# Kernel tuning notes

Hardware: AMD Instinct MI355X
Metric: run time of the kernel (lower is better)

The kernel has to match this reference:

```python
import jax, jax.numpy as jnp
import numpy as np

M, N = 8192, 8192
BITS = 3
BETA1, BETA2 = 16, 16
NNZ_PER_ROW = 32


def setup_inputs() -> dict:
    key = jax.random.key(0)
    ks = jax.random.split(key, 10)
    tm, tn = M // BETA1, N // BETA2
    nnz = M * NNZ_PER_ROW
    x = jax.random.normal(ks[0], (1, 10, N), dtype=jnp.float32)
    # quantized weight codes and first-order quantized scale/zero codes (3-bit)
    W = jax.random.randint(ks[1], (M, N), 0, 2 ** BITS, dtype=jnp.int32)
    W_s = jax.random.randint(ks[2], (M, tn), 0, 2 ** BITS, dtype=jnp.int32)
    W_z = jax.random.randint(ks[3], (M, tn), 0, 2 ** BITS, dtype=jnp.int32)
    # second-order (per-tile) float scale/zero for the quantized scales/zeros
    W_s_s = jax.random.uniform(ks[4], (tm, tn), jnp.float32, 0.01, 0.1)
    W_s_z = jax.random.uniform(ks[5], (tm, tn), jnp.float32, 0.0, 1.0)
    W_z_s = jax.random.uniform(ks[6], (tm, tn), jnp.float32, 0.01, 0.1)
    W_z_z = jax.random.uniform(ks[7], (tm, tn), jnp.float32, 0.0, 1.0)
    # CSR outliers: fixed 32 nnz per row
    row_offsets = jnp.arange(M + 1, dtype=jnp.int32) * NNZ_PER_ROW
    col_ids = jax.random.randint(ks[8], (nnz,), 0, N, dtype=jnp.int32)
    values = jax.random.normal(ks[9], (nnz,), dtype=jnp.float32)
    return dict(x=x, W=W, W_s=W_s, W_z=W_z, W_s_s=W_s_s, W_s_z=W_s_z,
                W_z_s=W_z_s, W_z_z=W_z_z, row_offsets=row_offsets,
                col_ids=col_ids, values=values)


def _dequantize(W, W_s, W_z, W_s_s, W_s_z, W_z_s, W_z_z):
    m, n = W.shape
    tm, tn = W_s_s.shape
    beta1, beta2 = m // tm, n // tn
    # two-level dequant: first-order scale/zero are themselves quantized per tile
    s = (W_s.astype(jnp.float32).reshape(tm, beta1, tn) - W_s_z[:, None, :]) * W_s_s[:, None, :]
    z = (W_z.astype(jnp.float32).reshape(tm, beta1, tn) - W_z_z[:, None, :]) * W_z_s[:, None, :]
    s = s.reshape(m, tn)  # (m, n/beta2)
    z = z.reshape(m, tn)
    w = (W.astype(jnp.float32).reshape(m, tn, beta2) - z[:, :, None]) * s[:, :, None]
    return w.reshape(m, n)


def reference(x, W, W_s, W_z, W_s_s, W_s_z, W_z_s, W_z_z, row_offsets, col_ids, values):
    Wd = _dequantize(W, W_s, W_z, W_s_s, W_s_z, W_z_s, W_z_z)  # (m, n)
    m = Wd.shape[0]
    b, l, n = x.shape
    xf = x.reshape(b * l, n)
    # dense quantized matmul: y = x @ Wd^T
    y = jnp.einsum('bn,mn->bm', xf, Wd)
    # CSR sparse outlier correction
    nnz = values.shape[0]
    rows = jnp.repeat(jnp.arange(m, dtype=jnp.int32), jnp.diff(row_offsets),
                      total_repeat_length=nnz)
    contrib = values[:, None] * xf[:, col_ids].T  # (nnz, B)
    y = y + jax.ops.segment_sum(contrib, rows, num_segments=m).T
    return y.reshape(b, l, m)
```

## Files before the change

### kernel.cpp

```cpp
#include <hip/hip_runtime.h>


constexpr int M_DIM = 8192;
constexpr int N_DIM = 8192;
constexpr int TN    = 512;
constexpr int BQ    = 10;
constexpr int RB    = 4;
constexpr int NTHREADS = 256;
constexpr int NC    = NTHREADS * 4;
constexpr int NCHUNK = N_DIM / NC;

__global__ __launch_bounds__(NTHREADS, 4)
void spqr_fused(const float* __restrict__ x,
                const int*   __restrict__ W,
                const int*   __restrict__ Ws,
                const int*   __restrict__ Wz,
                const float* __restrict__ Wss,
                const float* __restrict__ Wsz,
                const float* __restrict__ Wzs,
                const float* __restrict__ Wzz,
                const int*   __restrict__ row_offsets,
                const int*   __restrict__ col_ids,
                const float* __restrict__ values,
                float*       __restrict__ y)
{
    const int t  = threadIdx.x;
    const int m0 = blockIdx.x * RB;

    float acc[RB][BQ];
    #pragma unroll
    for (int r = 0; r < RB; ++r)
        #pragma unroll
        for (int b = 0; b < BQ; ++b)
            acc[r][b] = 0.f;

    for (int chunk = 0; chunk < NCHUNK; ++chunk) {
        const int n0 = chunk * NC + t * 4;
        float4 xv[BQ];
        #pragma unroll
        for (int b = 0; b < BQ; ++b)
            xv[b] = *reinterpret_cast<const float4*>(x + b * N_DIM + n0);

        const int g = n0 >> 4;

        #pragma unroll
        for (int r = 0; r < RB; ++r) {
            const int m  = m0 + r;
            const int ti = m >> 4;
            const int tIdx = ti * TN + g;
            const float s = ((float)Ws[m * TN + g] - Wsz[tIdx]) * Wss[tIdx];
            const float z = ((float)Wz[m * TN + g] - Wzz[tIdx]) * Wzs[tIdx];
            const int4 wc = *reinterpret_cast<const int4*>(W + (size_t)m * N_DIM + n0);
            const float w0 = ((float)wc.x - z) * s;
            const float w1 = ((float)wc.y - z) * s;
            const float w2 = ((float)wc.z - z) * s;
            const float w3 = ((float)wc.w - z) * s;
            #pragma unroll
            for (int b = 0; b < BQ; ++b) {
                float a = acc[r][b];
                a = fmaf(w0, xv[b].x, a);
                a = fmaf(w1, xv[b].y, a);
                a = fmaf(w2, xv[b].z, a);
                a = fmaf(w3, xv[b].w, a);
                acc[r][b] = a;
            }
        }
    }

    #pragma unroll
    for (int r = 0; r < RB; ++r)
        #pragma unroll
        for (int b = 0; b < BQ; ++b) {
            float v = acc[r][b];
            for (int off = 32; off > 0; off >>= 1)
                v += __shfl_xor(v, off, 64);
            acc[r][b] = v;
        }

    __shared__ float lds_part[NTHREADS / 64][RB * BQ];
    __shared__ float lds_sp[RB][BQ];

    const int wave = t >> 6;
    const int lane = t & 63;
    if (lane == 0) {
        #pragma unroll
        for (int r = 0; r < RB; ++r)
            #pragma unroll
            for (int b = 0; b < BQ; ++b)
                lds_part[wave][r * BQ + b] = acc[r][b];
    }
    if (t < RB * BQ)
        lds_sp[t / BQ][t % BQ] = 0.f;
    __syncthreads();

    if (t < RB * 32) {
        const int r = t >> 5;
        const int j = t & 31;
        const int m = m0 + r;
        const int base = row_offsets[m];
        const int cnt  = row_offsets[m + 1] - base;
        float c[BQ];
        #pragma unroll
        for (int b = 0; b < BQ; ++b) c[b] = 0.f;
        for (int jj = j; jj < cnt; jj += 32) {
            const int   col = col_ids[base + jj];
            const float v   = values[base + jj];
            #pragma unroll
            for (int b = 0; b < BQ; ++b)
                c[b] = fmaf(v, x[b * N_DIM + col], c[b]);
        }
        #pragma unroll
        for (int b = 0; b < BQ; ++b) {
            float v = c[b];
            for (int off = 16; off > 0; off >>= 1)
                v += __shfl_xor(v, off, 32);
            c[b] = v;
        }
        if (j == 0) {
            #pragma unroll
            for (int b = 0; b < BQ; ++b)
                lds_sp[r][b] = c[b];
        }
    }
    __syncthreads();

    if (t < RB * BQ) {
        const int r = t / BQ;
        const int b = t % BQ;
        float v = lds_sp[r][b];
        #pragma unroll
        for (int w = 0; w < NTHREADS / 64; ++w)
            v += lds_part[w][r * BQ + b];
        y[b * M_DIM + (m0 + r)] = v;
    }
}

extern "C" void kernel_launch(void* const* d_in, const int* in_sizes, int n_in,
                              void* d_out, int out_size, void* d_ws, size_t ws_size,
                              hipStream_t stream)
{
    const float* x    = (const float*)d_in[0];
    const int*   W    = (const int*)  d_in[1];
    const int*   Ws   = (const int*)  d_in[2];
    const int*   Wz   = (const int*)  d_in[3];
    const float* Wss  = (const float*)d_in[4];
    const float* Wsz  = (const float*)d_in[5];
    const float* Wzs  = (const float*)d_in[6];
    const float* Wzz  = (const float*)d_in[7];
    const int*   roff = (const int*)  d_in[8];
    const int*   cids = (const int*)  d_in[9];
    const float* vals = (const float*)d_in[10];
    float* yout = (float*)d_out;

    dim3 grid(M_DIM / RB);
    dim3 block(NTHREADS);
    spqr_fused<<<grid, block, 0, stream>>>(x, W, Ws, Wz, Wss, Wsz, Wzs, Wzz,
                                           roff, cids, vals, yout);
}
```

Baseline: 83.61 us.

## Process eight rows per block, hoist tile scales, restructure cross-thread reduction

Doubles the rows per block from 4 to 8 so each loaded x chunk is reused across more weight rows, and lowers the launch-bounds occupancy hint to allow more registers. Since 8 rows sit in one 16-row tile, the four second-order scale/zero loads are hoisted out of the row loop. The final reduction swaps the full 64-lane shuffle tree for a 2-step shuffle plus an LDS transpose reduction, and now all 256 threads run the sparse outlier pass. The cost is higher register pressure, lower occupancy, and half as many blocks.

```diff
diff --git a/kernel.cpp b/kernel.cpp
--- a/kernel.cpp
+++ b/kernel.cpp
@@ -5,12 +5,13 @@
 constexpr int N_DIM = 8192;
 constexpr int TN    = 512;
 constexpr int BQ    = 10;
-constexpr int RB    = 4;
+constexpr int RB    = 8;
 constexpr int NTHREADS = 256;
 constexpr int NC    = NTHREADS * 4;
 constexpr int NCHUNK = N_DIM / NC;
+constexpr int NOUT  = RB * BQ;
 
-__global__ __launch_bounds__(NTHREADS, 4)
+__global__ __launch_bounds__(NTHREADS, 2)
 void spqr_fused(const float* __restrict__ x,
                 const int*   __restrict__ W,
                 const int*   __restrict__ Ws,
@@ -26,6 +27,7 @@
 {
     const int t  = threadIdx.x;
     const int m0 = blockIdx.x * RB;
+    const int ti = m0 >> 4;
 
     float acc[RB][BQ];
     #pragma unroll
@@ -34,22 +36,29 @@
         for (int b = 0; b < BQ; ++b)
             acc[r][b] = 0.f;
 
+    const int tq = t * 4;
+
+    #pragma unroll 2
     for (int chunk = 0; chunk < NCHUNK; ++chunk) {
-        const int n0 = chunk * NC + t * 4;
+        const int n0 = chunk * NC + tq;
+        const int g  = n0 >> 4;
+        const int tIdx = ti * TN + g;
+
+        const float wss = Wss[tIdx];
+        const float wsz = Wsz[tIdx];
+        const float wzs = Wzs[tIdx];
+        const float wzz = Wzz[tIdx];
+
         float4 xv[BQ];
         #pragma unroll
         for (int b = 0; b < BQ; ++b)
             xv[b] = *reinterpret_cast<const float4*>(x + b * N_DIM + n0);
 
-        const int g = n0 >> 4;
-
         #pragma unroll
         for (int r = 0; r < RB; ++r) {
-            const int m  = m0 + r;
-            const int ti = m >> 4;
-            const int tIdx = ti * TN + g;
-            const float s = ((float)Ws[m * TN + g] - Wsz[tIdx]) * Wss[tIdx];
-            const float z = ((float)Wz[m * TN + g] - Wzz[tIdx]) * Wzs[tIdx];
+            const int m = m0 + r;
+            const float s = ((float)Ws[m * TN + g] - wsz) * wss;
+            const float z = ((float)Wz[m * TN + g] - wzz) * wzs;
             const int4 wc = *reinterpret_cast<const int4*>(W + (size_t)m * N_DIM + n0);
             const float w0 = ((float)wc.x - z) * s;
             const float w1 = ((float)wc.y - z) * s;
@@ -67,33 +76,8 @@
         }
     }
 
-    #pragma unroll
-    for (int r = 0; r < RB; ++r)
-        #pragma unroll
-        for (int b = 0; b < BQ; ++b) {
-            float v = acc[r][b];
-            for (int off = 32; off > 0; off >>= 1)
-                v += __shfl_xor(v, off, 64);
-            acc[r][b] = v;
-        }
-
-    __shared__ float lds_part[NTHREADS / 64][RB * BQ];
-    __shared__ float lds_sp[RB][BQ];
-
-    const int wave = t >> 6;
-    const int lane = t & 63;
-    if (lane == 0) {
-        #pragma unroll
-        for (int r = 0; r < RB; ++r)
-            #pragma unroll
-            for (int b = 0; b < BQ; ++b)
-                lds_part[wave][r * BQ + b] = acc[r][b];
-    }
-    if (t < RB * BQ)
-        lds_sp[t / BQ][t % BQ] = 0.f;
-    __syncthreads();
-
-    if (t < RB * 32) {
+    __shared__ float lsp[RB][BQ];
+    {
         const int r = t >> 5;
         const int j = t & 31;
         const int m = m0 + r;
@@ -119,19 +103,47 @@
         if (j == 0) {
             #pragma unroll
             for (int b = 0; b < BQ; ++b)
-                lds_sp[r][b] = c[b];
+                lsp[r][b] = c[b];
         }
+    }
+
+    #pragma unroll
+    for (int r = 0; r < RB; ++r)
+        #pragma unroll
+        for (int b = 0; b < BQ; ++b) {
+            float v = acc[r][b];
+            v += __shfl_xor(v, 1, 64);
+            v += __shfl_xor(v, 2, 64);
+            acc[r][b] = v;
+        }
+
+    __shared__ float lred[64][NOUT + 1];
+    if ((t & 3) == 0) {
+        const int q = t >> 2;
+        #pragma unroll
+        for (int r = 0; r < RB; ++r)
+            #pragma unroll
+            for (int b = 0; b < BQ; ++b)
+                lred[q][r * BQ + b] = acc[r][b];
+    }
+    __shared__ float l2[NOUT][2];
+    __syncthreads();
+
+    if (t < 2 * NOUT) {
+        const int out = t % NOUT;
+        const int h   = t / NOUT;
+        float v = 0.f;
+        #pragma unroll
+        for (int q = 0; q < 32; ++q)
+            v += lred[h * 32 + q][out];
+        l2[out][h] = v;
     }
     __syncthreads();
 
-    if (t < RB * BQ) {
+    if (t < NOUT) {
         const int r = t / BQ;
         const int b = t % BQ;
-        float v = lds_sp[r][b];
-        #pragma unroll
-        for (int w = 0; w < NTHREADS / 64; ++w)
-            v += lds_part[w][r * BQ + b];
-        y[b * M_DIM + (m0 + r)] = v;
+        y[b * M_DIM + (m0 + r)] = l2[t][0] + l2[t][1] + lsp[r][b];
     }
 }
 
```

New measurement: 107.7 us. 28.8% more time.

## Use bf16 MFMA with split-K partials and separate sparse/reduce kernel

Applied to the files above, without the earlier changes.

The fused FP32 GEMV is replaced by a kernel that dequantizes weights to bf16 and runs 16x16x32 MFMA instructions. x is staged into LDS as bf16 and the per-group scale/zero values are precomputed into LDS. The K dimension is split 16 ways into a workspace of partial sums. A second kernel adds the CSR outlier correction and reduces the partials. This cuts the FP32 ALU work and adds parallelism along K, at the cost of bf16 rounding of x and the weights, a second launch, and extra workspace traffic.

```diff
diff --git a/kernel.cpp b/kernel.cpp
--- a/kernel.cpp
+++ b/kernel.cpp
@@ -5,97 +5,133 @@
 constexpr int N_DIM = 8192;
 constexpr int TN    = 512;
 constexpr int BQ    = 10;
-constexpr int RB    = 4;
-constexpr int NTHREADS = 256;
-constexpr int NC    = NTHREADS * 4;
-constexpr int NCHUNK = N_DIM / NC;
+constexpr int KSPLIT = 16;
+constexpr int KRANGE = N_DIM / KSPLIT;
+constexpr int KITERS = KRANGE / 32;
+constexpr int RPB    = 64;
+constexpr int GPB    = KRANGE / 16;
 
-__global__ __launch_bounds__(NTHREADS, 4)
-void spqr_fused(const float* __restrict__ x,
-                const int*   __restrict__ W,
-                const int*   __restrict__ Ws,
-                const int*   __restrict__ Wz,
-                const float* __restrict__ Wss,
-                const float* __restrict__ Wsz,
-                const float* __restrict__ Wzs,
-                const float* __restrict__ Wzz,
-                const int*   __restrict__ row_offsets,
-                const int*   __restrict__ col_ids,
-                const float* __restrict__ values,
-                float*       __restrict__ y)
+typedef float  f32x4  __attribute__((ext_vector_type(4)));
+typedef float  f32x2  __attribute__((ext_vector_type(2)));
+typedef int    i32x4  __attribute__((ext_vector_type(4)));
+typedef short  bf16x8 __attribute__((ext_vector_type(8)));
+
+__device__ inline ushort f2bf(float f) {
+    unsigned u = __float_as_uint(f);
+    u += 0x7fffu + ((u >> 16) & 1u);
+    return (ushort)(u >> 16);
+}
+
+__global__ __launch_bounds__(256, 4)
+void spqr_mfma(const float* __restrict__ x,
+               const int*   __restrict__ W,
+               const int*   __restrict__ Ws,
+               const int*   __restrict__ Wz,
+               const float* __restrict__ Wss,
+               const float* __restrict__ Wsz,
+               const float* __restrict__ Wzs,
+               const float* __restrict__ Wzz,
+               float*       __restrict__ pws)
 {
-    const int t  = threadIdx.x;
-    const int m0 = blockIdx.x * RB;
+    __shared__ int   ldsA[KITERS * 64 * 4];
+    __shared__ f32x2 ldsSZ[RPB * 33];
 
-    float acc[RB][BQ];
+    const int t   = threadIdx.x;
+    const int m0b = blockIdx.x * RPB;
+    const int ks  = blockIdx.y;
+    const int k0  = ks * KRANGE;
+    const int g0  = k0 >> 4;
+
+    for (int idx = t; idx < KITERS * 64; idx += 256) {
+        const int kk = idx >> 6, l = idx & 63;
+        const int b = l & 15, koff = (kk << 5) + ((l >> 4) << 3);
+        int out[4] = {0, 0, 0, 0};
+        if (b < BQ) {
+            const float* xp = x + b * N_DIM + k0 + koff;
+            f32x4 lo = *reinterpret_cast<const f32x4*>(xp);
+            f32x4 hi = *reinterpret_cast<const f32x4*>(xp + 4);
+            out[0] = f2bf(lo.x) | ((unsigned)f2bf(lo.y) << 16);
+            out[1] = f2bf(lo.z) | ((unsigned)f2bf(lo.w) << 16);
+            out[2] = f2bf(hi.x) | ((unsigned)f2bf(hi.y) << 16);
+            out[3] = f2bf(hi.z) | ((unsigned)f2bf(hi.w) << 16);
+        }
+        *reinterpret_cast<i32x4*>(&ldsA[idx * 4]) = *reinterpret_cast<i32x4*>(out);
+    }
+
+    for (int idx = t; idx < RPB * GPB; idx += 256) {
+        const int rl = idx >> 5;
+        const int gl = idx & 31;
+        const int m = m0b + rl, g = g0 + gl;
+        const int tix = (m >> 4) * TN + g;
+        const float s = ((float)Ws[m * TN + g] - Wsz[tix]) * Wss[tix];
+        const float z = ((float)Wz[m * TN + g] - Wzz[tix]) * Wzs[tix];
+        ldsSZ[rl * 33 + gl] = (f32x2){s, z};
+    }
+    __syncthreads();
+
+    const int wv = t >> 6, l = t & 63;
+    const int lrow = l & 15;
+    const int lk   = l >> 4;
+    const int m0   = m0b + (wv << 4);
+    const int* wp  = W + (size_t)(m0 + lrow) * N_DIM + k0 + (lk << 3);
+    const int szrow = (wv << 4) + lrow;
+    const int szk   = lk >> 1;
+
+    f32x4 acc = {0.f, 0.f, 0.f, 0.f};
+    i32x4 cbufL[4], cbufH[4];
+
     #pragma unroll
-    for (int r = 0; r < RB; ++r)
-        #pragma unroll
-        for (int b = 0; b < BQ; ++b)
-            acc[r][b] = 0.f;
-
-    for (int chunk = 0; chunk < NCHUNK; ++chunk) {
-        const int n0 = chunk * NC + t * 4;
-        float4 xv[BQ];
-        #pragma unroll
-        for (int b = 0; b < BQ; ++b)
-            xv[b] = *reinterpret_cast<const float4*>(x + b * N_DIM + n0);
-
-        const int g = n0 >> 4;
-
-        #pragma unroll
-        for (int r = 0; r < RB; ++r) {
-            const int m  = m0 + r;
-            const int ti = m >> 4;
-            const int tIdx = ti * TN + g;
-            const float s = ((float)Ws[m * TN + g] - Wsz[tIdx]) * Wss[tIdx];
-            const float z = ((float)Wz[m * TN + g] - Wzz[tIdx]) * Wzs[tIdx];
-            const int4 wc = *reinterpret_cast<const int4*>(W + (size_t)m * N_DIM + n0);
-            const float w0 = ((float)wc.x - z) * s;
-            const float w1 = ((float)wc.y - z) * s;
-            const float w2 = ((float)wc.z - z) * s;
-            const float w3 = ((float)wc.w - z) * s;
-            #pragma unroll
-            for (int b = 0; b < BQ; ++b) {
-                float a = acc[r][b];
-                a = fmaf(w0, xv[b].x, a);
-                a = fmaf(w1, xv[b].y, a);
-                a = fmaf(w2, xv[b].z, a);
-                a = fmaf(w3, xv[b].w, a);
-                acc[r][b] = a;
-            }
-        }
+    for (int p = 0; p < 3; ++p) {
+        cbufL[p] = *reinterpret_cast<const i32x4*>(wp + p * 32);
+        cbufH[p] = *reinterpret_cast<const i32x4*>(wp + p * 32 + 4);
     }
 
     #pragma unroll
-    for (int r = 0; r < RB; ++r)
+    for (int kk = 0; kk < KITERS; ++kk) {
+        if (kk + 3 < KITERS) {
+            cbufL[(kk + 3) & 3] = *reinterpret_cast<const i32x4*>(wp + (kk + 3) * 32);
+            cbufH[(kk + 3) & 3] = *reinterpret_cast<const i32x4*>(wp + (kk + 3) * 32 + 4);
+        }
+        const i32x4 a4 = *reinterpret_cast<const i32x4*>(&ldsA[(kk * 64 + l) * 4]);
+        const f32x2 sz = ldsSZ[szrow * 33 + kk * 2 + szk];
+        const float s  = sz.x;
+        const float nzs = -sz.y * sz.x;
+        const i32x4 cl = cbufL[kk & 3], ch = cbufH[kk & 3];
+        const int c[8] = {cl.x, cl.y, cl.z, cl.w, ch.x, ch.y, ch.z, ch.w};
+        int bw[4];
         #pragma unroll
-        for (int b = 0; b < BQ; ++b) {
-            float v = acc[r][b];
-            for (int off = 32; off > 0; off >>= 1)
-                v += __shfl_xor(v, off, 64);
-            acc[r][b] = v;
+        for (int d = 0; d < 4; ++d) {
+            const float w0 = fmaf((float)c[2 * d],     s, nzs);
+            const float w1 = fmaf((float)c[2 * d + 1], s, nzs);
+            bw[d] = f2bf(w0) | ((unsigned)f2bf(w1) << 16);
         }
+        const bf16x8 af = __builtin_bit_cast(bf16x8, a4);
+        const bf16x8 bf = __builtin_bit_cast(bf16x8, *reinterpret_cast<i32x4*>(bw));
+        acc = __builtin_amdgcn_mfma_f32_16x16x32_bf16(af, bf, acc, 0, 0, 0);
+    }
 
-    __shared__ float lds_part[NTHREADS / 64][RB * BQ];
-    __shared__ float lds_sp[RB][BQ];
+    float* pb = pws + (size_t)ks * (BQ * N_DIM) + (m0 + lrow);
+    #pragma unroll
+    for (int j = 0; j < 4; ++j) {
+        const int b = (lk << 2) + j;
+        if (b < BQ) pb[(size_t)b * N_DIM] = acc[j];
+    }
+}
 
-    const int wave = t >> 6;
-    const int lane = t & 63;
-    if (lane == 0) {
-        #pragma unroll
-        for (int r = 0; r < RB; ++r)
-            #pragma unroll
-            for (int b = 0; b < BQ; ++b)
-                lds_part[wave][r * BQ + b] = acc[r][b];
-    }
-    if (t < RB * BQ)
-        lds_sp[t / BQ][t % BQ] = 0.f;
-    __syncthreads();
+__global__ __launch_bounds__(256, 4)
+void spqr_reduce(const float* __restrict__ x,
+                 const int*   __restrict__ row_offsets,
+                 const int*   __restrict__ col_ids,
+                 const float* __restrict__ values,
+                 const float* __restrict__ pws,
+                 float*       __restrict__ y)
+{
+    __shared__ float lsp[8][BQ];
+    const int t  = threadIdx.x;
+    const int m0 = blockIdx.x * 8;
 
-    if (t < RB * 32) {
-        const int r = t >> 5;
-        const int j = t & 31;
+    {
+        const int r = t >> 5, j = t & 31;
         const int m = m0 + r;
         const int base = row_offsets[m];
         const int cnt  = row_offsets[m + 1] - base;
@@ -118,20 +154,20 @@
         }
         if (j == 0) {
             #pragma unroll
-            for (int b = 0; b < BQ; ++b)
-                lds_sp[r][b] = c[b];
+            for (int b = 0; b < BQ; ++b) lsp[r][b] = c[b];
         }
     }
     __syncthreads();
 
-    if (t < RB * BQ) {
-        const int r = t / BQ;
-        const int b = t % BQ;
-        float v = lds_sp[r][b];
+    if (t < 8 * BQ) {
+        const int ml = t / BQ, b = t % BQ;
+        const int m = m0 + ml;
+        float v = lsp[ml][b];
+        const float* pp = pws + (size_t)b * N_DIM + m;
         #pragma unroll
-        for (int w = 0; w < NTHREADS / 64; ++w)
-            v += lds_part[w][r * BQ + b];
-        y[b * M_DIM + (m0 + r)] = v;
+        for (int ksp = 0; ksp < KSPLIT; ++ksp)
+            v += pp[(size_t)ksp * (BQ * N_DIM)];
+        y[(size_t)b * M_DIM + m] = v;
     }
 }
 
@@ -151,9 +187,11 @@
     const int*   cids = (const int*)  d_in[9];
     const float* vals = (const float*)d_in[10];
     float* yout = (float*)d_out;
+    float* pws  = (float*)d_ws;
 
-    dim3 grid(M_DIM / RB);
-    dim3 block(NTHREADS);
-    spqr_fused<<<grid, block, 0, stream>>>(x, W, Ws, Wz, Wss, Wsz, Wzs, Wzz,
-                                           roff, cids, vals, yout);
+    dim3 grid1(M_DIM / RPB, KSPLIT);
+    spqr_mfma<<<grid1, dim3(256), 0, stream>>>(x, W, Ws, Wz, Wss, Wsz, Wzs, Wzz, pws);
+
+    dim3 grid2(M_DIM / 8);
+    spqr_reduce<<<grid2, dim3(256), 0, stream>>>(x, roff, cids, vals, pws, yout);
 }
```

Result: faster. 79.17 us (-5.3%).
